# Optimization experiments

Hardware: AMD Instinct MI355X
Metric: run time of the kernel (lower is better)

## Reference

```python
import jax, jax.numpy as jnp
import numpy as np

B, N, IMG, CH, HID, LENA = 32, 64, 144, 16, 32, 6
EPS = 1e-5
DN = ('NCHW', 'OIHW', 'NCHW')


def _bn(y, g, b, m, v):
    # eval-mode batchnorm over channel dim of [BN, C, h, w]
    inv = jax.lax.rsqrt(v + EPS)
    return (y - m[None, :, None, None]) * (g * inv)[None, :, None, None] + b[None, :, None, None]


def _pool3(y):
    return jax.lax.reduce_window(y, -jnp.inf, jax.lax.max, (1, 1, 3, 3), (1, 1, 3, 3), 'VALID')


def setup_inputs() -> dict:
    key = jax.random.key(0)
    ks = jax.random.split(key, 24)
    r = lambda i, shape, s=0.1: (jax.random.normal(ks[i], shape, dtype=jnp.float32) * s)
    inp = {
        'x': jax.random.normal(ks[0], (B, N, 3, IMG, IMG), dtype=jnp.float32),
        'conv1_w': r(1, (CH, 3, 4, 4)),
        'conv1_b': r(2, (CH,)),
        'bn1_g': 1.0 + r(3, (CH,)),
        'bn1_b': r(4, (CH,)),
        'bn1_m': jnp.zeros((CH,), jnp.float32),
        'bn1_v': jnp.ones((CH,), jnp.float32),
        'conv2_w': r(5, (1, CH, 4, 4)),
        'conv2_b': r(6, (1,)),
        'bn2_g': 1.0 + r(7, (1,)),
        'bn2_b': r(8, (1,)),
        'bn2_m': jnp.zeros((1,), jnp.float32),
        'bn2_v': jnp.ones((1,), jnp.float32),
        'pre_w1': r(9, (32, N)),
        'pre_b1': r(10, (32,)),
        'pre_w2': r(11, (32, 32)),
        'pre_b2': r(12, (32,)),
        'pre_w3': r(13, (LENA, 32)),
        'pre_b3': r(14, (LENA,)),
        'lstm_wih': r(15, (LENA, 4 * HID, 1)),
        'lstm_whh': r(16, (LENA, 4 * HID, HID)),
        'lstm_bih': r(17, (LENA, 4 * HID)),
        'lstm_bhh': r(18, (LENA, 4 * HID)),
        'hn0': jnp.zeros((LENA, HID), jnp.float32),
        'out_w': r(19, (LENA, N)),
        'out_b': r(20, (LENA,)),
    }
    return inp


def reference(x, conv1_w, conv1_b, bn1_g, bn1_b, bn1_m, bn1_v,
              conv2_w, conv2_b, bn2_g, bn2_b, bn2_m, bn2_v,
              pre_w1, pre_b1, pre_w2, pre_b2, pre_w3, pre_b3,
              lstm_wih, lstm_whh, lstm_bih, lstm_bhh, hn0, out_w, out_b):
    Bb, Nn = x.shape[0], x.shape[1]
    f = x.reshape(Bb * Nn, 3, IMG, IMG)
    y = jax.lax.conv_general_dilated(f, conv1_w, (4, 4), 'VALID', dimension_numbers=DN)
    y = y + conv1_b[None, :, None, None]
    y = _pool3(jax.nn.relu(_bn(y, bn1_g, bn1_b, bn1_m, bn1_v)))          # [BN,CH,12,12]
    y = jax.lax.conv_general_dilated(y, conv2_w, (4, 4), 'VALID', dimension_numbers=DN)
    y = y + conv2_b[None, :, None, None]
    y = _pool3(jax.nn.relu(_bn(y, bn2_g, bn2_b, bn2_m, bn2_v)))          # [BN,1,1,1]
    c = y.reshape(Bb, Nn)                                                # one scalar per frame

    # gating MLP (softmax then argmax -> hard expert index)
    h = jnp.tanh(c @ pre_w1.T + pre_b1)
    h = jnp.tanh(h @ pre_w2.T + pre_b2)
    probs = jax.nn.softmax(h @ pre_w3.T + pre_b3, axis=1)
    p = jnp.argmax(probs, axis=1)                                        # [B]

    seq = c[..., None]                                                   # [B,N,1]

    def sample_step(hn_tab, inp):
        pi, s = inp
        wih = lstm_wih[pi]                                               # [4H,1]
        whh = lstm_whh[pi]                                               # [4H,H]
        bsum = lstm_bih[pi] + lstm_bhh[pi]
        h0 = hn_tab[pi]

        def cell(carry, xt):
            hh, cc = carry
            g = wih @ xt + whh @ hh + bsum
            i_g, f_g, g_g, o_g = jnp.split(g, 4)
            cc2 = jax.nn.sigmoid(f_g) * cc + jax.nn.sigmoid(i_g) * jnp.tanh(g_g)
            hh2 = jax.nn.sigmoid(o_g) * jnp.tanh(cc2)
            return (hh2, cc2), hh2[-1]                                   # o[:, -1]: last hidden unit per step

        (hN, _), outs = jax.lax.scan(cell, (h0, jnp.zeros_like(h0)), s)
        return hn_tab.at[pi].set(hN), outs                               # stateful hn update chains across batch

    _, r = jax.lax.scan(sample_step, hn0, (p, seq))                      # r [B,N]
    return r @ out_w.T + out_b                                           # [B,lenA]
```

## Files before the change

### kernel.cpp

```cpp
#include <hip/hip_runtime.h>

#define EPS 1e-5f

__device__ __forceinline__ float fast_rcp(float x) { return __builtin_amdgcn_rcpf(x); }
__device__ __forceinline__ float sigm(float x) { return fast_rcp(1.f + __expf(-x)); }
__device__ __forceinline__ float tanh_fast(float x) { return 1.f - 2.f * fast_rcp(1.f + __expf(2.f * x)); }
__device__ __forceinline__ float rdlane(float v, int l) {
    return __int_as_float(__builtin_amdgcn_readlane(__float_as_int(v), l));
}

__global__ __launch_bounds__(256, 4) void kAB(
    const float* __restrict__ x,
    const float* __restrict__ w1, const float* __restrict__ cb1,
    const float* __restrict__ g1, const float* __restrict__ b1,
    const float* __restrict__ m1, const float* __restrict__ v1,
    const float* __restrict__ w2, const float* __restrict__ cb2,
    const float* __restrict__ g2, const float* __restrict__ b2,
    const float* __restrict__ m2, const float* __restrict__ v2,
    float* __restrict__ c)
{
    __shared__ float sc[16], sh[16];
    __shared__ float convbuf[6][36][17];
    __shared__ float plds[16][12][13];

    const int tid = threadIdx.x;
    const int img = blockIdx.x;
    const float* xb = x + (size_t)img * 62208;

    if (tid < 16) {
        float s = g1[tid] * rsqrtf(v1[tid] + EPS);
        sc[tid] = s;
        sh[tid] = b1[tid] + (cb1[tid] - m1[tid]) * s;
    }
    __syncthreads();

    for (int pp = 0; pp < 6; ++pp) {
        if (tid < 216) {
            const int ox = tid % 36;
            const int ry = tid / 36;
            const int oy = pp * 6 + ry;
            const float* pbase = xb + oy * 576 + ox * 4;
            float4 patch[12];
#pragma unroll
            for (int ci = 0; ci < 3; ++ci)
#pragma unroll
                for (int dy = 0; dy < 4; ++dy)
                    patch[ci * 4 + dy] = *(const float4*)(pbase + ci * 20736 + dy * 144);
            float acc[16];
#pragma unroll
            for (int co = 0; co < 16; ++co) acc[co] = 0.f;
#pragma unroll
            for (int q = 0; q < 12; ++q) {
                const float4 pq = patch[q];
#pragma unroll
                for (int co = 0; co < 16; ++co) {
                    const float* wp = w1 + co * 48 + q * 4;
                    acc[co] = fmaf(pq.x, wp[0],
                              fmaf(pq.y, wp[1],
                              fmaf(pq.z, wp[2],
                              fmaf(pq.w, wp[3], acc[co]))));
                }
            }
#pragma unroll
            for (int co = 0; co < 16; ++co)
                convbuf[ry][ox][co] = fmaxf(fmaf(acc[co], sc[co], sh[co]), 0.f);
        }
        __syncthreads();
        for (int i = tid; i < 384; i += 256) {
            const int pr = i & 1;
            const int px = (i >> 1) % 12;
            const int co = i / 24;
            float best = 0.f;
#pragma unroll
            for (int dy = 0; dy < 3; ++dy)
#pragma unroll
                for (int dx = 0; dx < 3; ++dx)
                    best = fmaxf(best, convbuf[pr * 3 + dy][px * 3 + dx][co]);
            plds[co][pp * 2 + pr][px] = best;
        }
        __syncthreads();
    }

    if (tid < 64) {
        const int ch = tid >> 2, dy = tid & 3;
        const float4 wv = *(const float4*)(w2 + ch * 16 + dy * 4);
        const float scale = g2[0] * rsqrtf(v2[0] + EPS);
        const float shift = b2[0] + (cb2[0] - m2[0]) * scale;
        float best = 0.f;
#pragma unroll
        for (int oy = 0; oy < 3; ++oy)
#pragma unroll
            for (int ox = 0; ox < 3; ++ox) {
                const float* ab = &plds[ch][4 * oy + dy][4 * ox];
                float s = ab[0] * wv.x + ab[1] * wv.y + ab[2] * wv.z + ab[3] * wv.w;
#pragma unroll
                for (int off = 32; off >= 1; off >>= 1) s += __shfl_xor(s, off);
                float val = fmaxf(fmaf(s, scale, shift), 0.f);
                best = fmaxf(best, val);
            }
        if (tid == 0) c[img] = best;
    }
}

__global__ __launch_bounds__(64) void kC(
    const float* __restrict__ c,
    const float* __restrict__ w1, const float* __restrict__ b1,
    const float* __restrict__ w2, const float* __restrict__ b2,
    const float* __restrict__ w3, const float* __restrict__ b3,
    int* __restrict__ p)
{
    const int b = threadIdx.x;
    if (b >= 32) return;
    const float* cb = c + b * 64;
    float h1[32];
#pragma unroll
    for (int j = 0; j < 32; ++j) {
        float s = b1[j];
        for (int i = 0; i < 64; ++i) s = fmaf(w1[j * 64 + i], cb[i], s);
        h1[j] = tanhf(s);
    }
    float h2[32];
#pragma unroll
    for (int j = 0; j < 32; ++j) {
        float s = b2[j];
#pragma unroll
        for (int i = 0; i < 32; ++i) s = fmaf(w2[j * 32 + i], h1[i], s);
        h2[j] = tanhf(s);
    }
    float best = -3.4e38f;
    int bi = 0;
#pragma unroll
    for (int j = 0; j < 6; ++j) {
        float s = b3[j];
#pragma unroll
        for (int i = 0; i < 32; ++i) s = fmaf(w3[j * 32 + i], h2[i], s);
        if (s > best) { best = s; bi = j; }
    }
    p[b] = bi;
}

__global__ __launch_bounds__(64, 1) void kD(
    const float* __restrict__ c, const int* __restrict__ p,
    const float* __restrict__ wih, const float* __restrict__ whh,
    const float* __restrict__ bih, const float* __restrict__ bhh,
    const float* __restrict__ hn0,
    const float* __restrict__ ow, const float* __restrict__ obias,
    float* __restrict__ out)
{
    const int e = blockIdx.x;
    const int lane = threadIdx.x;
    const int k = lane & 31;
    const float* we = whh + e * 4096;

    float4 wI4[8], wF4[8], wG4[8], wO4[8];
#pragma unroll
    for (int j = 0; j < 8; ++j) {
        wI4[j] = *(const float4*)(we + (k)      * 32 + j * 4);
        wF4[j] = *(const float4*)(we + (k + 32) * 32 + j * 4);
        wG4[j] = *(const float4*)(we + (k + 64) * 32 + j * 4);
        wO4[j] = *(const float4*)(we + (k + 96) * 32 + j * 4);
    }
    const float wiI = wih[e * 128 + k],      wiF = wih[e * 128 + k + 32];
    const float wiG = wih[e * 128 + k + 64], wiO = wih[e * 128 + k + 96];
    const float bI = bih[e * 128 + k]      + bhh[e * 128 + k];
    const float bF = bih[e * 128 + k + 32] + bhh[e * 128 + k + 32];
    const float bG = bih[e * 128 + k + 64] + bhh[e * 128 + k + 64];
    const float bO = bih[e * 128 + k + 96] + bhh[e * 128 + k + 96];
    float h = hn0[e * 32 + k];

    for (int b = 0; b < 32; ++b) {
        if (p[b] != e) continue;
        const float cvec = c[b * 64 + lane];
        float cc = 0.f;
        float rvec = 0.f;
        for (int t = 0; t < 64; ++t) {
            const float xt = rdlane(cvec, t);
            float aI0 = fmaf(wiI, xt, bI), aI1 = 0.f;
            float aF0 = fmaf(wiF, xt, bF), aF1 = 0.f;
            float aG0 = fmaf(wiG, xt, bG), aG1 = 0.f;
            float aO0 = fmaf(wiO, xt, bO), aO1 = 0.f;
#pragma unroll
            for (int j = 0; j < 8; ++j) {
                const float h0 = rdlane(h, 4 * j + 0);
                const float h1 = rdlane(h, 4 * j + 1);
                const float h2 = rdlane(h, 4 * j + 2);
                const float h3 = rdlane(h, 4 * j + 3);
                aI0 = fmaf(wI4[j].x, h0, aI0); aI1 = fmaf(wI4[j].y, h1, aI1);
                aI0 = fmaf(wI4[j].z, h2, aI0); aI1 = fmaf(wI4[j].w, h3, aI1);
                aF0 = fmaf(wF4[j].x, h0, aF0); aF1 = fmaf(wF4[j].y, h1, aF1);
                aF0 = fmaf(wF4[j].z, h2, aF0); aF1 = fmaf(wF4[j].w, h3, aF1);
                aG0 = fmaf(wG4[j].x, h0, aG0); aG1 = fmaf(wG4[j].y, h1, aG1);
                aG0 = fmaf(wG4[j].z, h2, aG0); aG1 = fmaf(wG4[j].w, h3, aG1);
                aO0 = fmaf(wO4[j].x, h0, aO0); aO1 = fmaf(wO4[j].y, h1, aO1);
                aO0 = fmaf(wO4[j].z, h2, aO0); aO1 = fmaf(wO4[j].w, h3, aO1);
            }
            const float ig = sigm(aI0 + aI1), fg = sigm(aF0 + aF1);
            const float gg = tanh_fast(aG0 + aG1), og = sigm(aO0 + aO1);
            cc = fmaf(fg, cc, ig * gg);
            h = og * tanh_fast(cc);
            const float h31 = rdlane(h, 31);
            rvec = (lane == t) ? h31 : rvec;
        }
#pragma unroll
        for (int a = 0; a < 6; ++a) {
            float tsum = rvec * ow[a * 64 + lane];
#pragma unroll
            for (int off = 32; off >= 1; off >>= 1) tsum += __shfl_xor(tsum, off);
            if (lane == 0) out[b * 6 + a] = tsum + obias[a];
        }
    }
}

extern "C" void kernel_launch(void* const* d_in, const int* in_sizes, int n_in,
                              void* d_out, int out_size, void* d_ws, size_t ws_size,
                              hipStream_t stream)
{
    const float* x    = (const float*)d_in[0];
    const float* c1w  = (const float*)d_in[1];
    const float* c1b  = (const float*)d_in[2];
    const float* bn1g = (const float*)d_in[3];
    const float* bn1b = (const float*)d_in[4];
    const float* bn1m = (const float*)d_in[5];
    const float* bn1v = (const float*)d_in[6];
    const float* c2w  = (const float*)d_in[7];
    const float* c2b  = (const float*)d_in[8];
    const float* bn2g = (const float*)d_in[9];
    const float* bn2b = (const float*)d_in[10];
    const float* bn2m = (const float*)d_in[11];
    const float* bn2v = (const float*)d_in[12];
    const float* pw1  = (const float*)d_in[13];
    const float* pb1  = (const float*)d_in[14];
    const float* pw2  = (const float*)d_in[15];
    const float* pb2  = (const float*)d_in[16];
    const float* pw3  = (const float*)d_in[17];
    const float* pb3  = (const float*)d_in[18];
    const float* wih  = (const float*)d_in[19];
    const float* whh  = (const float*)d_in[20];
    const float* bihp = (const float*)d_in[21];
    const float* bhhp = (const float*)d_in[22];
    const float* hn0  = (const float*)d_in[23];
    const float* ow   = (const float*)d_in[24];
    const float* ob   = (const float*)d_in[25];
    float* out = (float*)d_out;

    float* c = (float*)d_ws;
    int*   p = (int*)((char*)d_ws + 2048 * sizeof(float));

    kAB<<<2048, 256, 0, stream>>>(x, c1w, c1b, bn1g, bn1b, bn1m, bn1v,
                                  c2w, c2b, bn2g, bn2b, bn2m, bn2v, c);
    kC<<<1, 64, 0, stream>>>(c, pw1, pb1, pw2, pb2, pw3, pb3, p);
    kD<<<6, 64, 0, stream>>>(c, p, wih, whh, bihp, bhhp, hn0, ow, ob, out);
}
```

Measured before the change: 1.426 ms.

## Split LSTM gate rows across both wave halves to halve per-lane FMA work

The LSTM recurrence kernel previously ran the same 32 hidden units duplicated on both halves of the 64-lane wave, each lane computing all four gate dot products. Now the lower half computes the input and forget gates and the upper half computes the cell-candidate and output gates. A unified sigmoid/tanh formula selected by per-half constants keeps the activation path branch-free, and a cross-half shuffle exchanges the results. This halves the FMAs and weight registers per lane on the serial critical path, but adds two cross-half shuffles per timestep, which may add latency.

Measured after the change: 1.373 ms. 1.04x faster.

```diff
diff --git a/kernel.cpp b/kernel.cpp
--- a/kernel.cpp
+++ b/kernel.cpp
@@ -150,22 +150,29 @@
     const int e = blockIdx.x;
     const int lane = threadIdx.x;
     const int k = lane & 31;
-    const float* we = whh + e * 4096;
-
-    float4 wI4[8], wF4[8], wG4[8], wO4[8];
-#pragma unroll
-    for (int j = 0; j < 8; ++j) {
-        wI4[j] = *(const float4*)(we + (k)      * 32 + j * 4);
-        wF4[j] = *(const float4*)(we + (k + 32) * 32 + j * 4);
-        wG4[j] = *(const float4*)(we + (k + 64) * 32 + j * 4);
-        wO4[j] = *(const float4*)(we + (k + 96) * 32 + j * 4);
-    }
-    const float wiI = wih[e * 128 + k],      wiF = wih[e * 128 + k + 32];
-    const float wiG = wih[e * 128 + k + 64], wiO = wih[e * 128 + k + 96];
-    const float bI = bih[e * 128 + k]      + bhh[e * 128 + k];
-    const float bF = bih[e * 128 + k + 32] + bhh[e * 128 + k + 32];
-    const float bG = bih[e * 128 + k + 64] + bhh[e * 128 + k + 64];
-    const float bO = bih[e * 128 + k + 96] + bhh[e * 128 + k + 96];
+    const int hf = lane >> 5;
+    const int rowA = k + (hf << 6);
+    const int rowB = rowA + 32;
+
+    const float* wa = whh + e * 4096 + rowA * 32;
+    const float* wb = whh + e * 4096 + rowB * 32;
+    const float4 a0 = *(const float4*)(wa +  0), a1 = *(const float4*)(wa +  4);
+    const float4 a2 = *(const float4*)(wa +  8), a3 = *(const float4*)(wa + 12);
+    const float4 a4 = *(const float4*)(wa + 16), a5 = *(const float4*)(wa + 20);
+    const float4 a6 = *(const float4*)(wa + 24), a7 = *(const float4*)(wa + 28);
+    const float4 b0 = *(const float4*)(wb +  0), b1 = *(const float4*)(wb +  4);
+    const float4 b2 = *(const float4*)(wb +  8), b3 = *(const float4*)(wb + 12);
+    const float4 b4 = *(const float4*)(wb + 16), b5 = *(const float4*)(wb + 20);
+    const float4 b6 = *(const float4*)(wb + 24), b7 = *(const float4*)(wb + 28);
+
+    const float wiA = wih[e * 128 + rowA], wiB = wih[e * 128 + rowB];
+    const float bA  = bih[e * 128 + rowA] + bhh[e * 128 + rowA];
+    const float bB  = bih[e * 128 + rowB] + bhh[e * 128 + rowB];
+
+    const float C1 = hf ? 1.f : 0.f;
+    const float C2 = hf ? -2.f : 1.f;
+    const float C3 = hf ? 2.f : -1.f;
+
     float h = hn0[e * 32 + k];
 
     for (int b = 0; b < 32; ++b) {
@@ -175,27 +182,30 @@
         float rvec = 0.f;
         for (int t = 0; t < 64; ++t) {
             const float xt = rdlane(cvec, t);
-            float aI0 = fmaf(wiI, xt, bI), aI1 = 0.f;
-            float aF0 = fmaf(wiF, xt, bF), aF1 = 0.f;
-            float aG0 = fmaf(wiG, xt, bG), aG1 = 0.f;
-            float aO0 = fmaf(wiO, xt, bO), aO1 = 0.f;
-#pragma unroll
-            for (int j = 0; j < 8; ++j) {
-                const float h0 = rdlane(h, 4 * j + 0);
-                const float h1 = rdlane(h, 4 * j + 1);
-                const float h2 = rdlane(h, 4 * j + 2);
-                const float h3 = rdlane(h, 4 * j + 3);
-                aI0 = fmaf(wI4[j].x, h0, aI0); aI1 = fmaf(wI4[j].y, h1, aI1);
-                aI0 = fmaf(wI4[j].z, h2, aI0); aI1 = fmaf(wI4[j].w, h3, aI1);
-                aF0 = fmaf(wF4[j].x, h0, aF0); aF1 = fmaf(wF4[j].y, h1, aF1);
-                aF0 = fmaf(wF4[j].z, h2, aF0); aF1 = fmaf(wF4[j].w, h3, aF1);
-                aG0 = fmaf(wG4[j].x, h0, aG0); aG1 = fmaf(wG4[j].y, h1, aG1);
-                aG0 = fmaf(wG4[j].z, h2, aG0); aG1 = fmaf(wG4[j].w, h3, aG1);
-                aO0 = fmaf(wO4[j].x, h0, aO0); aO1 = fmaf(wO4[j].y, h1, aO1);
-                aO0 = fmaf(wO4[j].z, h2, aO0); aO1 = fmaf(wO4[j].w, h3, aO1);
-            }
-            const float ig = sigm(aI0 + aI1), fg = sigm(aF0 + aF1);
-            const float gg = tanh_fast(aG0 + aG1), og = sigm(aO0 + aO1);
+            float A0 = fmaf(wiA, xt, bA), A1 = 0.f;
+            float B0 = fmaf(wiB, xt, bB), B1 = 0.f;
+#define GRP(q, av, bv) { \
+            const float h0 = rdlane(h, 4*q + 0); \
+            const float h1 = rdlane(h, 4*q + 1); \
+            const float h2 = rdlane(h, 4*q + 2); \
+            const float h3 = rdlane(h, 4*q + 3); \
+            A0 = fmaf(av.x, h0, A0); A1 = fmaf(av.y, h1, A1); \
+            A0 = fmaf(av.z, h2, A0); A1 = fmaf(av.w, h3, A1); \
+            B0 = fmaf(bv.x, h0, B0); B1 = fmaf(bv.y, h1, B1); \
+            B0 = fmaf(bv.z, h2, B0); B1 = fmaf(bv.w, h3, B1); }
+            GRP(0, a0, b0) GRP(1, a1, b1) GRP(2, a2, b2) GRP(3, a3, b3)
+            GRP(4, a4, b4) GRP(5, a5, b5) GRP(6, a6, b6) GRP(7, a7, b7)
+#undef GRP
+            const float accA = A0 + A1;
+            const float accB = B0 + B1;
+            const float actA = fmaf(C2, fast_rcp(1.f + __expf(C3 * accA)), C1);
+            const float actB = fast_rcp(1.f + __expf(-accB));
+            const float xA = __shfl_xor(actA, 32);
+            const float xB = __shfl_xor(actB, 32);
+            const float ig = hf ? xA   : actA;
+            const float fg = hf ? xB   : actB;
+            const float gg = hf ? actA : xA;
+            const float og = hf ? actB : xB;
             cc = fmaf(fg, cc, ig * gg);
             h = og * tanh_fast(cc);
             const float h31 = rdlane(h, 31);
```
